# Performance work log

Hardware: AMD Instinct MI355X
Metric: run time of the kernel (lower is better)

The kernel has to match this reference:

```python
import jax, jax.numpy as jnp
import numpy as np

B, T, DP, A = 1024, 256, 64, 8   # batch, num particles (seq len), particle dim, action dim
H = 256                          # recurr_size (GRU hidden)
HID = 256                        # MLP hidden
C = 2                            # num_critics
TIME_NORM = 100.0


def setup_inputs() -> dict:
    key = jax.random.key(0)
    ks = jax.random.split(key, 10)
    F = DP + 1        # features + weight channel
    DIN = H + A + 1   # encoding + action + time
    s = lambda k, shape: (jax.random.normal(k, shape, jnp.float32) * 0.05)
    return {
        "particles": jax.random.normal(ks[0], (B, T, DP), jnp.float32),
        "weights": jax.random.uniform(ks[1], (B, T), jnp.float32),
        "action": jax.random.normal(ks[2], (B, A), jnp.float32),
        "time_idx": jax.random.uniform(ks[3], (B,), jnp.float32) * TIME_NORM,
        # GRU params (flax GRUCell layout, gates fused as [r|z|n]):
        "Wi": s(ks[4], (F, 3 * H)),    # input kernel (ir|iz|in), with bias
        "bi": jnp.zeros((3 * H,), jnp.float32),
        "Wh": s(ks[5], (H, 3 * H)),    # hidden kernel (hr|hz|hn); only hn has bias
        "bhn": jnp.zeros((H,), jnp.float32),
        # Two MLPDecoder critics stacked on leading dim C:
        "W1": s(ks[6], (C, DIN, HID)),
        "b1": jnp.zeros((C, HID), jnp.float32),
        "W2": s(ks[7], (C, HID, HID)),
        "b2": jnp.zeros((C, HID), jnp.float32),
        "W3": s(ks[8], (C, HID, 1)),
        "b3": jnp.zeros((C, 1), jnp.float32),
    }


def reference(particles, weights, action, time_idx, Wi, bi, Wh, bhn, W1, b1, W2, b2, W3, b3):
    # feature_fn = identity; append particle weights as an extra channel
    inputs = jnp.concatenate([particles, weights[..., None]], axis=-1)  # [B,T,F]
    # Precompute all input projections (parallel over time), scan only the recurrence.
    xp = jnp.einsum('btf,fg->btg', inputs, Wi) + bi                     # [B,T,3H]
    xp = jnp.swapaxes(xp, 0, 1)                                         # [T,B,3H]
    h0 = jnp.zeros((inputs.shape[0], H), inputs.dtype)

    def step(h, x):
        hp = h @ Wh                                                     # [B,3H]
        r = jax.nn.sigmoid(x[:, :H] + hp[:, :H])
        z = jax.nn.sigmoid(x[:, H:2 * H] + hp[:, H:2 * H])
        n = jnp.tanh(x[:, 2 * H:] + r * (hp[:, 2 * H:] + bhn))
        h_new = (1.0 - z) * n + z * h
        return h_new, None

    h, _ = jax.lax.scan(step, h0, xp)                                   # last encoding [B,H]

    t = (time_idx / TIME_NORM)[:, None]                                 # [B,1]
    x = jnp.concatenate([h, action, t], axis=-1)                        # [B,DIN]

    # Both critic MLPs batched over leading critic dim C (ReLU hidden layers).
    h1 = jax.nn.relu(jnp.einsum('bd,cdh->cbh', x, W1) + b1[:, None, :])   # [C,B,HID]
    h2 = jax.nn.relu(jnp.einsum('cbh,chk->cbk', h1, W2) + b2[:, None, :]) # [C,B,HID]
    v = jnp.einsum('cbh,cho->cbo', h2, W3) + b3[:, None, :]               # [C,B,1]
    return jnp.moveaxis(v[..., 0], 0, -1)                               # [B,C]
```

## Files before the change

### kernel.cpp

```cpp
#include <hip/hip_runtime.h>


#define TSEQ 256
#define DPDIM 64

typedef float f32x4 __attribute__((ext_vector_type(4)));
typedef __bf16 bf16x8 __attribute__((ext_vector_type(8)));
typedef unsigned short ushort8 __attribute__((ext_vector_type(8)));

static __device__ __forceinline__ unsigned short f2bf(float f) {
  unsigned u = __builtin_bit_cast(unsigned, f);
  return (unsigned short)((u + 0x7fffu + ((u >> 16) & 1u)) >> 16);
}
static __device__ __forceinline__ float bf2f(unsigned short h) {
  return __builtin_bit_cast(float, ((unsigned)h) << 16);
}
static __device__ __forceinline__ float sigm(float x) {
  return __builtin_amdgcn_rcpf(1.f + __expf(-x));
}
static __device__ __forceinline__ float tanh_fast(float p) {
  float q = __expf(-2.f * fabsf(p));
  float t = (1.f - q) * __builtin_amdgcn_rcpf(1.f + q);
  return __builtin_bit_cast(float, __builtin_bit_cast(unsigned, t) |
                                   (__builtin_bit_cast(unsigned, p) & 0x80000000u));
}

#define OFF_WIT 0
#define OFF_XP  110592
#define OFF_H0  135168
#define OFF_H1  137888
#define OFF_BI  140608
#define OFF_W64 143680
#define OFF_BHN 146752
#define LDS_GRU 147776

#define HSTRIDE 544

__global__ __launch_bounds__(512, 2) void gru_kernel(
    const float* __restrict__ particles, const float* __restrict__ weights,
    const float* __restrict__ Wi, const float* __restrict__ bi,
    const float* __restrict__ Wh, const float* __restrict__ bhn,
    unsigned short* __restrict__ hT)
{
  extern __shared__ char smem[];
  const int tid  = threadIdx.x;
  const int lane = tid & 63;
  const int w    = tid >> 6;
  const int l15  = lane & 15;
  const int kg   = lane >> 4;
  const int b0   = blockIdx.x * 4;

  for (int idx = tid; idx < 64 * 768; idx += 512) {
    int k = idx / 768, n = idx - k * 768;
    *(unsigned short*)(smem + OFF_WIT + n * 144 + k * 2) = f2bf(Wi[idx]);
  }
  for (int idx = tid; idx < 768; idx += 512) {
    *(float*)(smem + OFF_BI  + idx * 4) = bi[idx];
    *(float*)(smem + OFF_W64 + idx * 4) = Wi[64 * 768 + idx];
  }
  if (tid < 256) *(float*)(smem + OFF_BHN + tid * 4) = bhn[tid];
  for (int idx = tid; idx < (2 * 5 * HSTRIDE) / 4; idx += 512)
    ((unsigned*)(smem + OFF_H0))[idx] = 0u;

  bf16x8 whb[6][8];
  #pragma unroll
  for (int j = 0; j < 6; ++j) {
    const int tile = w + 8 * j;
    const float* wp = Wh + (size_t)(kg * 8) * 768 + tile * 16 + l15;
    #pragma unroll
    for (int ks = 0; ks < 8; ++ks) {
      ushort8 tmp;
      #pragma unroll
      for (int e = 0; e < 8; ++e)
        tmp[e] = f2bf(wp[(size_t)(ks * 32 + e) * 768]);
      whb[j][ks] = __builtin_bit_cast(bf16x8, tmp);
    }
  }
  __syncthreads();

  const unsigned arow = ((l15 & 3) == 0)
                      ? (unsigned)((l15 >> 2) * HSTRIDE + kg * 16)
                      : (unsigned)(4 * HSTRIDE + kg * 16);

  f32x4 acc[6];
  const f32x4 fzero = {0.f, 0.f, 0.f, 0.f};

  for (int g = 0; g < 64; ++g) {
    const int t0 = g * 4;

    float wv[4];
    #pragma unroll
    for (int r = 0; r < 4; ++r) {
      int row = kg * 4 + r;
      wv[r] = weights[(b0 + (row & 3)) * TSEQ + t0 + (row >> 2)];
    }
    #pragma unroll
    for (int j = 0; j < 6; ++j) acc[j] = fzero;
    #pragma unroll
    for (int ks = 0; ks < 2; ++ks) {
      const float* pp = particles +
          ((size_t)(b0 + (l15 & 3)) * TSEQ + (t0 + (l15 >> 2))) * DPDIM + ks * 32 + kg * 8;
      f32x4 pa = *(const f32x4*)pp;
      f32x4 pb = *(const f32x4*)(pp + 4);
      ushort8 tmp;
      tmp[0] = f2bf(pa[0]); tmp[1] = f2bf(pa[1]); tmp[2] = f2bf(pa[2]); tmp[3] = f2bf(pa[3]);
      tmp[4] = f2bf(pb[0]); tmp[5] = f2bf(pb[1]); tmp[6] = f2bf(pb[2]); tmp[7] = f2bf(pb[3]);
      bf16x8 af = __builtin_bit_cast(bf16x8, tmp);
      #pragma unroll
      for (int j = 0; j < 6; ++j) {
        const int n = (w + 8 * j) * 16 + l15;
        bf16x8 bf = *(const bf16x8*)(smem + OFF_WIT + n * 144 + ks * 64 + kg * 16);
        acc[j] = __builtin_amdgcn_mfma_f32_16x16x32_bf16(af, bf, acc[j], 0, 0, 0);
      }
    }
    #pragma unroll
    for (int j = 0; j < 6; ++j) {
      const int col  = (w + 8 * j) * 16 + l15;
      const float biv = *(const float*)(smem + OFF_BI  + col * 4);
      const float w64 = *(const float*)(smem + OFF_W64 + col * 4);
      float v0 = acc[j][0] + biv + wv[0] * w64;
      float v1 = acc[j][1] + biv + wv[1] * w64;
      float v2 = acc[j][2] + biv + wv[2] * w64;
      float v3 = acc[j][3] + biv + wv[3] * w64;
      uint2 val;
      val.x = (unsigned)f2bf(v0) | ((unsigned)f2bf(v1) << 16);
      val.y = (unsigned)f2bf(v2) | ((unsigned)f2bf(v3) << 16);
      *(uint2*)(smem + OFF_XP + col * 32 + kg * 8) = val;
    }

    #pragma unroll
    for (int tt = 0; tt < 4; ++tt) {
      const int t     = t0 + tt;
      const int rboff = (t & 1) ? OFF_H1 : OFF_H0;
      const int wboff = (t & 1) ? OFF_H0 : OFF_H1;
      #pragma unroll
      for (int j = 0; j < 6; ++j) acc[j] = fzero;
      const char* hb = smem + rboff;
      #pragma unroll
      for (int ks = 0; ks < 8; ++ks) {
        bf16x8 af = *(const bf16x8*)(hb + arow + ks * 64);
        #pragma unroll
        for (int j = 0; j < 6; ++j)
          acc[j] = __builtin_amdgcn_mfma_f32_16x16x32_bf16(af, whb[j][ks], acc[j], 0, 0, 0);
      }
      const int m = 4 * tt + kg;
      #pragma unroll
      for (int p = 0; p < 2; ++p) {
        const int hcol = (w + 8 * p) * 16 + l15;
        const float bhv = *(const float*)(smem + OFF_BHN + hcol * 4);
        float xr = bf2f(*(const unsigned short*)(smem + OFF_XP + (hcol      ) * 32 + m * 2));
        float xz = bf2f(*(const unsigned short*)(smem + OFF_XP + (hcol + 256) * 32 + m * 2));
        float xn = bf2f(*(const unsigned short*)(smem + OFF_XP + (hcol + 512) * 32 + m * 2));
        float rr = sigm(xr + acc[p][0]);
        float zz = sigm(xz + acc[2 + p][0]);
        float nn = tanh_fast(xn + rr * (acc[4 + p][0] + bhv));
        float ho = bf2f(*(const unsigned short*)(smem + rboff + kg * HSTRIDE + hcol * 2));
        *(unsigned short*)(smem + wboff + kg * HSTRIDE + hcol * 2) =
            f2bf(nn + zz * (ho - nn));
      }
      __syncthreads();
    }
  }

  for (int idx = tid; idx < 1024; idx += 512) {
    int b = idx >> 8, k = idx & 255;
    hT[(b0 + b) * 256 + k] = *(const unsigned short*)(smem + OFF_H0 + b * HSTRIDE + k * 2);
  }
}

#define HOFF_XA 0
#define HOFF_B  37888
#define HOFF_H1 58368
#define HOFF_H2 92160
#define HOFF_B1 125952
#define HOFF_B2 126976
#define HOFF_W3 128000
#define LDS_HEAD 129024

__global__ __launch_bounds__(256, 2) void head_kernel(
    const unsigned short* __restrict__ hT, const float* __restrict__ action,
    const float* __restrict__ time_idx, const float* __restrict__ W1,
    const float* __restrict__ b1, const float* __restrict__ W2,
    const float* __restrict__ b2, const float* __restrict__ W3,
    const float* __restrict__ b3, float* __restrict__ out)
{
  extern __shared__ char smem[];
  const int tid  = threadIdx.x;
  const int lane = tid & 63;
  const int w    = tid >> 6;
  const int l15  = lane & 15;
  const int kg   = lane >> 4;
  const int c    = blockIdx.x & 1;
  const int rt   = blockIdx.x >> 1;
  const int r0   = rt * 64;

  if (tid < 256) {
    *(float*)(smem + HOFF_B1 + tid * 4) = b1[c * 256 + tid];
    *(float*)(smem + HOFF_B2 + tid * 4) = b2[c * 256 + tid];
    *(float*)(smem + HOFF_W3 + tid * 4) = W3[c * 256 + tid];
  }
  for (int idx = tid; idx < 64 * 296; idx += 256) {
    int row = idx / 296, k = idx - row * 296;
    unsigned short v;
    if (k < 256)       v = hT[(r0 + row) * 256 + k];
    else if (k < 264)  v = f2bf(action[(r0 + row) * 8 + (k - 256)]);
    else if (k == 264) v = f2bf(time_idx[r0 + row] * 0.01f);
    else               v = 0;
    *(unsigned short*)(smem + HOFF_XA + row * 592 + k * 2) = v;
  }

  f32x4 acc[4][4];
  const f32x4 fzero = {0.f, 0.f, 0.f, 0.f};

  #pragma unroll
  for (int mt = 0; mt < 4; ++mt)
    #pragma unroll
    for (int i = 0; i < 4; ++i) acc[mt][i] = fzero;
  for (int ks = 0; ks < 9; ++ks) {
    for (int idx = tid; idx < 32 * 256; idx += 256) {
      int kk = idx >> 8, n = idx & 255;
      int kglob = ks * 32 + kk;
      float v = (kglob < 265) ? W1[((size_t)c * 265 + kglob) * 256 + n] : 0.f;
      *(unsigned short*)(smem + HOFF_B + n * 80 + kk * 2) = f2bf(v);
    }
    __syncthreads();
    bf16x8 bfr[4];
    #pragma unroll
    for (int i = 0; i < 4; ++i)
      bfr[i] = *(const bf16x8*)(smem + HOFF_B + ((w * 4 + i) * 16 + l15) * 80 + kg * 16);
    #pragma unroll
    for (int mt = 0; mt < 4; ++mt) {
      bf16x8 af = *(const bf16x8*)(smem + HOFF_XA + (mt * 16 + l15) * 592 + ks * 64 + kg * 16);
      #pragma unroll
      for (int i = 0; i < 4; ++i)
        acc[mt][i] = __builtin_amdgcn_mfma_f32_16x16x32_bf16(af, bfr[i], acc[mt][i], 0, 0, 0);
    }
    __syncthreads();
  }
  #pragma unroll
  for (int mt = 0; mt < 4; ++mt)
    #pragma unroll
    for (int i = 0; i < 4; ++i) {
      int col = (w * 4 + i) * 16 + l15;
      float bv = *(const float*)(smem + HOFF_B1 + col * 4);
      #pragma unroll
      for (int r = 0; r < 4; ++r) {
        float v = acc[mt][i][r] + bv; v = v > 0.f ? v : 0.f;
        *(unsigned short*)(smem + HOFF_H1 + (mt * 16 + kg * 4 + r) * 528 + col * 2) = f2bf(v);
      }
    }
  __syncthreads();

  #pragma unroll
  for (int mt = 0; mt < 4; ++mt)
    #pragma unroll
    for (int i = 0; i < 4; ++i) acc[mt][i] = fzero;
  for (int ks = 0; ks < 8; ++ks) {
    for (int idx = tid; idx < 32 * 256; idx += 256) {
      int kk = idx >> 8, n = idx & 255;
      float v = W2[((size_t)c * 256 + ks * 32 + kk) * 256 + n];
      *(unsigned short*)(smem + HOFF_B + n * 80 + kk * 2) = f2bf(v);
    }
    __syncthreads();
    bf16x8 bfr[4];
    #pragma unroll
    for (int i = 0; i < 4; ++i)
      bfr[i] = *(const bf16x8*)(smem + HOFF_B + ((w * 4 + i) * 16 + l15) * 80 + kg * 16);
    #pragma unroll
    for (int mt = 0; mt < 4; ++mt) {
      bf16x8 af = *(const bf16x8*)(smem + HOFF_H1 + (mt * 16 + l15) * 528 + ks * 64 + kg * 16);
      #pragma unroll
      for (int i = 0; i < 4; ++i)
        acc[mt][i] = __builtin_amdgcn_mfma_f32_16x16x32_bf16(af, bfr[i], acc[mt][i], 0, 0, 0);
    }
    __syncthreads();
  }
  #pragma unroll
  for (int mt = 0; mt < 4; ++mt)
    #pragma unroll
    for (int i = 0; i < 4; ++i) {
      int col = (w * 4 + i) * 16 + l15;
      float bv = *(const float*)(smem + HOFF_B2 + col * 4);
      #pragma unroll
      for (int r = 0; r < 4; ++r) {
        float v = acc[mt][i][r] + bv; v = v > 0.f ? v : 0.f;
        *(unsigned short*)(smem + HOFF_H2 + (mt * 16 + kg * 4 + r) * 528 + col * 2) = f2bf(v);
      }
    }
  __syncthreads();

  {
    int row = tid >> 2, q = tid & 3;
    float s = 0.f;
    #pragma unroll
    for (int i = 0; i < 16; ++i) {
      uint2 hh = *(const uint2*)(smem + HOFF_H2 + row * 528 + (q * 64 + i * 4) * 2);
      const float* w3p = (const float*)(smem + HOFF_W3) + q * 64 + i * 4;
      s += bf2f((unsigned short)hh.x)         * w3p[0];
      s += bf2f((unsigned short)(hh.x >> 16)) * w3p[1];
      s += bf2f((unsigned short)hh.y)         * w3p[2];
      s += bf2f((unsigned short)(hh.y >> 16)) * w3p[3];
    }
    s += __shfl_xor(s, 1);
    s += __shfl_xor(s, 2);
    if (q == 0) out[(r0 + row) * 2 + c] = s + b3[c];
  }
}

extern "C" void kernel_launch(void* const* d_in, const int* in_sizes, int n_in,
                              void* d_out, int out_size, void* d_ws, size_t ws_size,
                              hipStream_t stream) {
  const float* particles = (const float*)d_in[0];
  const float* weights   = (const float*)d_in[1];
  const float* action    = (const float*)d_in[2];
  const float* time_idx  = (const float*)d_in[3];
  const float* Wi        = (const float*)d_in[4];
  const float* bi        = (const float*)d_in[5];
  const float* Wh        = (const float*)d_in[6];
  const float* bhn       = (const float*)d_in[7];
  const float* W1        = (const float*)d_in[8];
  const float* b1        = (const float*)d_in[9];
  const float* W2        = (const float*)d_in[10];
  const float* b2        = (const float*)d_in[11];
  const float* W3        = (const float*)d_in[12];
  const float* b3        = (const float*)d_in[13];
  unsigned short* hT = (unsigned short*)d_ws;
  float* out = (float*)d_out;

  (void)hipFuncSetAttribute((const void*)gru_kernel,
                            hipFuncAttributeMaxDynamicSharedMemorySize, LDS_GRU);
  (void)hipFuncSetAttribute((const void*)head_kernel,
                            hipFuncAttributeMaxDynamicSharedMemorySize, LDS_HEAD);

  hipLaunchKernelGGL(gru_kernel, dim3(256), dim3(512), LDS_GRU, stream,
                     particles, weights, Wi, bi, Wh, bhn, hT);
  hipLaunchKernelGGL(head_kernel, dim3(32), dim3(256), LDS_HEAD, stream,
                     hT, action, time_idx, W1, b1, W2, b2, W3, b3, out);
}
```

Measured before the change: 758.8 us.

## Keep GRU input projections and hidden state in registers, prefetch particles

Changes the input-projection MFMA layout so each lane's accumulator lines up with the gate columns and timesteps it later consumes. The xp LDS staging buffer and its bf16 round trip go away, and bias, weight-channel and bhn values are held in registers. The previous hidden value is also kept in a register instead of being reread from LDS. Particle and weight loads for the next 4-step group are prefetched to overlap global latency with the recurrence, at the cost of more register pressure.

Measured after the change: 1.696 ms. +123.5%, slower.

```diff
diff --git a/kernel.cpp b/kernel.cpp
--- a/kernel.cpp
+++ b/kernel.cpp
@@ -26,13 +26,9 @@
 }
 
 #define OFF_WIT 0
-#define OFF_XP  110592
-#define OFF_H0  135168
-#define OFF_H1  137888
-#define OFF_BI  140608
-#define OFF_W64 143680
-#define OFF_BHN 146752
-#define LDS_GRU 147776
+#define OFF_H0  110592
+#define OFF_H1  113312
+#define LDS_GRU 116032
 
 #define HSTRIDE 544
 
@@ -54,13 +50,19 @@
     int k = idx / 768, n = idx - k * 768;
     *(unsigned short*)(smem + OFF_WIT + n * 144 + k * 2) = f2bf(Wi[idx]);
   }
-  for (int idx = tid; idx < 768; idx += 512) {
-    *(float*)(smem + OFF_BI  + idx * 4) = bi[idx];
-    *(float*)(smem + OFF_W64 + idx * 4) = Wi[64 * 768 + idx];
-  }
-  if (tid < 256) *(float*)(smem + OFF_BHN + tid * 4) = bhn[tid];
   for (int idx = tid; idx < (2 * 5 * HSTRIDE) / 4; idx += 512)
     ((unsigned*)(smem + OFF_H0))[idx] = 0u;
+
+  const int hcol0 = w * 16 + l15;
+  float bi_r[6], w64_r[6];
+  #pragma unroll
+  for (int j = 0; j < 6; ++j) {
+    const int col = hcol0 + 128 * j;
+    bi_r[j]  = bi[col];
+    w64_r[j] = Wi[64 * 768 + col];
+  }
+  const float bhn0 = bhn[hcol0];
+  const float bhn1 = bhn[hcol0 + 128];
 
   bf16x8 whb[6][8];
   #pragma unroll
@@ -82,51 +84,56 @@
                       ? (unsigned)((l15 >> 2) * HSTRIDE + kg * 16)
                       : (unsigned)(4 * HSTRIDE + kg * 16);
 
-  f32x4 acc[6];
+  const float* pbase = particles +
+      ((size_t)(b0 + (l15 >> 2)) * TSEQ + (l15 & 3)) * DPDIM + kg * 8;
+  const float* wbase = weights + (size_t)(b0 + kg) * TSEQ;
+
+  f32x4 pr[4], wv;
+  pr[0] = *(const f32x4*)(pbase);
+  pr[1] = *(const f32x4*)(pbase + 4);
+  pr[2] = *(const f32x4*)(pbase + 32);
+  pr[3] = *(const f32x4*)(pbase + 36);
+  wv    = *(const f32x4*)(wbase);
+
+  f32x4 acc[6], acc2[6];
   const f32x4 fzero = {0.f, 0.f, 0.f, 0.f};
+  float hreg0 = 0.f, hreg1 = 0.f;
 
   for (int g = 0; g < 64; ++g) {
     const int t0 = g * 4;
 
-    float wv[4];
-    #pragma unroll
-    for (int r = 0; r < 4; ++r) {
-      int row = kg * 4 + r;
-      wv[r] = weights[(b0 + (row & 3)) * TSEQ + t0 + (row >> 2)];
-    }
-    #pragma unroll
-    for (int j = 0; j < 6; ++j) acc[j] = fzero;
+    #pragma unroll
+    for (int j = 0; j < 6; ++j) acc2[j] = fzero;
     #pragma unroll
     for (int ks = 0; ks < 2; ++ks) {
-      const float* pp = particles +
-          ((size_t)(b0 + (l15 & 3)) * TSEQ + (t0 + (l15 >> 2))) * DPDIM + ks * 32 + kg * 8;
-      f32x4 pa = *(const f32x4*)pp;
-      f32x4 pb = *(const f32x4*)(pp + 4);
+      f32x4 pa = pr[ks * 2], pb = pr[ks * 2 + 1];
       ushort8 tmp;
       tmp[0] = f2bf(pa[0]); tmp[1] = f2bf(pa[1]); tmp[2] = f2bf(pa[2]); tmp[3] = f2bf(pa[3]);
       tmp[4] = f2bf(pb[0]); tmp[5] = f2bf(pb[1]); tmp[6] = f2bf(pb[2]); tmp[7] = f2bf(pb[3]);
       bf16x8 af = __builtin_bit_cast(bf16x8, tmp);
       #pragma unroll
       for (int j = 0; j < 6; ++j) {
-        const int n = (w + 8 * j) * 16 + l15;
+        const int n = hcol0 + 128 * j;
         bf16x8 bf = *(const bf16x8*)(smem + OFF_WIT + n * 144 + ks * 64 + kg * 16);
-        acc[j] = __builtin_amdgcn_mfma_f32_16x16x32_bf16(af, bf, acc[j], 0, 0, 0);
+        acc2[j] = __builtin_amdgcn_mfma_f32_16x16x32_bf16(af, bf, acc2[j], 0, 0, 0);
       }
     }
-    #pragma unroll
-    for (int j = 0; j < 6; ++j) {
-      const int col  = (w + 8 * j) * 16 + l15;
-      const float biv = *(const float*)(smem + OFF_BI  + col * 4);
-      const float w64 = *(const float*)(smem + OFF_W64 + col * 4);
-      float v0 = acc[j][0] + biv + wv[0] * w64;
-      float v1 = acc[j][1] + biv + wv[1] * w64;
-      float v2 = acc[j][2] + biv + wv[2] * w64;
-      float v3 = acc[j][3] + biv + wv[3] * w64;
-      uint2 val;
-      val.x = (unsigned)f2bf(v0) | ((unsigned)f2bf(v1) << 16);
-      val.y = (unsigned)f2bf(v2) | ((unsigned)f2bf(v3) << 16);
-      *(uint2*)(smem + OFF_XP + col * 32 + kg * 8) = val;
-    }
+
+    {
+      const int t0n = (g < 63) ? (t0 + 4) : 0;
+      const float* pn = pbase + (size_t)t0n * DPDIM;
+      pr[0] = *(const f32x4*)(pn);
+      pr[1] = *(const f32x4*)(pn + 4);
+      pr[2] = *(const f32x4*)(pn + 32);
+      pr[3] = *(const f32x4*)(pn + 36);
+    }
+    f32x4 wvn = *(const f32x4*)(wbase + ((g < 63) ? (t0 + 4) : 0));
+
+    #pragma unroll
+    for (int j = 0; j < 6; ++j)
+      #pragma unroll
+      for (int r = 0; r < 4; ++r)
+        acc2[j][r] += bi_r[j] + wv[r] * w64_r[j];
 
     #pragma unroll
     for (int tt = 0; tt < 4; ++tt) {
@@ -143,29 +150,25 @@
         for (int j = 0; j < 6; ++j)
           acc[j] = __builtin_amdgcn_mfma_f32_16x16x32_bf16(af, whb[j][ks], acc[j], 0, 0, 0);
       }
-      const int m = 4 * tt + kg;
-      #pragma unroll
-      for (int p = 0; p < 2; ++p) {
-        const int hcol = (w + 8 * p) * 16 + l15;
-        const float bhv = *(const float*)(smem + OFF_BHN + hcol * 4);
-        float xr = bf2f(*(const unsigned short*)(smem + OFF_XP + (hcol      ) * 32 + m * 2));
-        float xz = bf2f(*(const unsigned short*)(smem + OFF_XP + (hcol + 256) * 32 + m * 2));
-        float xn = bf2f(*(const unsigned short*)(smem + OFF_XP + (hcol + 512) * 32 + m * 2));
-        float rr = sigm(xr + acc[p][0]);
-        float zz = sigm(xz + acc[2 + p][0]);
-        float nn = tanh_fast(xn + rr * (acc[4 + p][0] + bhv));
-        float ho = bf2f(*(const unsigned short*)(smem + rboff + kg * HSTRIDE + hcol * 2));
-        *(unsigned short*)(smem + wboff + kg * HSTRIDE + hcol * 2) =
-            f2bf(nn + zz * (ho - nn));
-      }
+      float rr0 = sigm(acc2[0][tt] + acc[0][0]);
+      float zz0 = sigm(acc2[2][tt] + acc[2][0]);
+      float nn0 = tanh_fast(acc2[4][tt] + rr0 * (acc[4][0] + bhn0));
+      unsigned short h0u = f2bf(nn0 + zz0 * (hreg0 - nn0));
+      hreg0 = bf2f(h0u);
+      float rr1 = sigm(acc2[1][tt] + acc[1][0]);
+      float zz1 = sigm(acc2[3][tt] + acc[3][0]);
+      float nn1 = tanh_fast(acc2[5][tt] + rr1 * (acc[5][0] + bhn1));
+      unsigned short h1u = f2bf(nn1 + zz1 * (hreg1 - nn1));
+      hreg1 = bf2f(h1u);
+      *(unsigned short*)(smem + wboff + kg * HSTRIDE + hcol0 * 2)         = h0u;
+      *(unsigned short*)(smem + wboff + kg * HSTRIDE + (hcol0 + 128) * 2) = h1u;
       __syncthreads();
     }
-  }
-
-  for (int idx = tid; idx < 1024; idx += 512) {
-    int b = idx >> 8, k = idx & 255;
-    hT[(b0 + b) * 256 + k] = *(const unsigned short*)(smem + OFF_H0 + b * HSTRIDE + k * 2);
-  }
+    wv = wvn;
+  }
+
+  hT[(size_t)(b0 + kg) * 256 + hcol0]       = f2bf(hreg0);
+  hT[(size_t)(b0 + kg) * 256 + hcol0 + 128] = f2bf(hreg1);
 }
 
 #define HOFF_XA 0
```
